# Kernel optimization log

Hardware: AMD Instinct MI355X
Metric: run time of the kernel (lower is better)

The kernel has to match this reference:

```python
import jax, jax.numpy as jnp
import numpy as np

N = 100_000
E = 1_250_000
D = 64
PAIRS = 3  # layer_num=3 -> 3 (SAGE, GIN) pairs
EPS = 1e-5


def _linear_init(key, fi, fo):
    lim = 1.0 / np.sqrt(fi)
    k1, k2 = jax.random.split(key)
    W = jax.random.uniform(k1, (fi, fo), minval=-lim, maxval=lim, dtype=jnp.float32)
    b = jax.random.uniform(k2, (fo,), minval=-lim, maxval=lim, dtype=jnp.float32)
    return W, b


def setup_inputs() -> dict:
    key = jax.random.key(0)
    ks = jax.random.split(key, 40)
    # graph
    src = jax.random.randint(ks[0], (E,), 0, N, dtype=jnp.int32)
    dst = jax.random.randint(ks[1], (E,), 0, N, dtype=jnp.int32)
    sign = (jax.random.randint(ks[2], (E,), 0, 2, dtype=jnp.int32) * 2 - 1)
    edge_index_s = jnp.stack([src, dst, sign], axis=1)  # [E,3]
    init_emb = jax.random.normal(ks[3], (N, D), dtype=jnp.float32)
    rate_b = jax.random.uniform(ks[4], (1,), dtype=jnp.float32)

    def stack_lin(kbase, fi, fo, n):
        Ws, bs = [], []
        for i in range(n):
            W, b = _linear_init(jax.random.fold_in(kbase, i), fi, fo)
            Ws.append(W); bs.append(b)
        return jnp.stack(Ws), jnp.stack(bs)

    sage_lin_W, sage_lin_b = stack_lin(ks[5], D, D, PAIRS)
    sage_norm_w = jnp.ones((PAIRS, D), jnp.float32)
    sage_norm_b = jnp.zeros((PAIRS, D), jnp.float32)
    rsW, rsB = stack_lin(ks[6], 1, D, PAIRS)   # rate_scale Linear(1,D)
    rbW, rbB = stack_lin(ks[7], 1, D, PAIRS)   # rate_bias Linear(1,D)
    sage_rs_w, sage_rs_b = rsW[:, 0, :], rsB   # [PAIRS,D]
    sage_rb_w, sage_rb_b = rbW[:, 0, :], rbB
    gin_W1, gin_b1 = stack_lin(ks[8], D, D, PAIRS)
    gin_W2, gin_b2 = stack_lin(ks[9], D, D, PAIRS)
    fuse_W, fuse_b = _linear_init(ks[10], 2 * PAIRS * D, D)
    ro_W1, ro_b1 = _linear_init(ks[11], D, 128)
    ro_W2, ro_b2 = _linear_init(ks[12], 128, 128)
    ro_W3, ro_b3 = _linear_init(ks[13], 128, 1)
    ro_ln1_g = jnp.ones((128,), jnp.float32); ro_ln1_b = jnp.zeros((128,), jnp.float32)
    ro_ln2_g = jnp.ones((128,), jnp.float32); ro_ln2_b = jnp.zeros((128,), jnp.float32)
    return dict(init_emb=init_emb, edge_index_s=edge_index_s, rate_b=rate_b,
                sage_lin_W=sage_lin_W, sage_lin_b=sage_lin_b,
                sage_norm_w=sage_norm_w, sage_norm_b=sage_norm_b,
                sage_rs_w=sage_rs_w, sage_rs_b=sage_rs_b,
                sage_rb_w=sage_rb_w, sage_rb_b=sage_rb_b,
                gin_W1=gin_W1, gin_b1=gin_b1, gin_W2=gin_W2, gin_b2=gin_b2,
                fuse_W=fuse_W, fuse_b=fuse_b,
                ro_W1=ro_W1, ro_b1=ro_b1, ro_ln1_g=ro_ln1_g, ro_ln1_b=ro_ln1_b,
                ro_W2=ro_W2, ro_b2=ro_b2, ro_ln2_g=ro_ln2_g, ro_ln2_b=ro_ln2_b,
                ro_W3=ro_W3, ro_b3=ro_b3)


def _graph_norm(x, w, b, rs_w, rs_b, rb_w, rb_b, rate):
    # batch stats over nodes (dim 0), biased variance
    mean = x.mean(0, keepdims=True)
    var = x.var(0, keepdims=True)
    x_norm = (x - mean) / jnp.sqrt(var + EPS)
    gamma = w + (rs_w * rate + rs_b)  # rate_scale(rate_b)
    beta = b + (rb_w * rate + rb_b)
    return x_norm * gamma + beta


def _layer_norm(v, g, b):
    m = v.mean(-1, keepdims=True)
    va = v.var(-1, keepdims=True)
    return (v - m) / jnp.sqrt(va + EPS) * g + b


def _forward(init_emb, edge_index_s, rate_b,
             sage_lin_W, sage_lin_b, sage_norm_w, sage_norm_b,
             sage_rs_w, sage_rs_b, sage_rb_w, sage_rb_b,
             gin_W1, gin_b1, gin_W2, gin_b2,
             fuse_W, fuse_b,
             ro_W1, ro_b1, ro_ln1_g, ro_ln1_b,
             ro_W2, ro_b2, ro_ln2_g, ro_ln2_b,
             ro_W3, ro_b3):
    n = init_emb.shape[0]
    src = edge_index_s[:, 0]
    dst = edge_index_s[:, 1]
    sign = edge_index_s[:, 2].astype(init_emb.dtype)
    rate = rate_b.reshape(())
    # degree including self-loop (for mean aggregation with fill_value=1 self loops)
    deg = jax.ops.segment_sum(jnp.ones_like(sign), dst, num_segments=n) + 1.0  # [n]
    gelu = lambda t: jax.nn.gelu(t, approximate=False)  # torch nn.GELU default = exact

    x = init_emb
    outputs = []
    for i in range(PAIRS):
        # --- StableEfficientEdgeSAGEConv (mean aggr, sign-scaled, self-loops, skip=Identity) ---
        xt = x @ sage_lin_W[i] + sage_lin_b[i]
        msg = sign[:, None] * xt[src]                                   # gather + sign scale
        agg = (jax.ops.segment_sum(msg, dst, num_segments=n) + xt) / deg[:, None]
        h = agg + x                                                     # skip (in==out -> Identity)
        h = _graph_norm(h, sage_norm_w[i], sage_norm_b[i],
                        sage_rs_w[i], sage_rs_b[i], sage_rb_w[i], sage_rb_b[i], rate)
        x = gelu(h)                                                     # dropout: eval mode (no-op)
        outputs.append(x)
        # --- GINConv (sum aggr, eps=0, no self-loops) mlp = Lin-GELU-Lin ---
        agg2 = jax.ops.segment_sum(x[src], dst, num_segments=n)
        z = x + agg2
        x = gelu(z @ gin_W1[i] + gin_b1[i]) @ gin_W2[i] + gin_b2[i]
        outputs.append(x)

    x_dense = jnp.concatenate(outputs, axis=1)          # [n, 6*D]
    x_final = x_dense @ fuse_W + fuse_b                 # [n, D]
    # readout MLP (2 hidden layers + head), eval-mode dropout
    hdd = jax.nn.relu(_layer_norm(x_final @ ro_W1 + ro_b1, ro_ln1_g, ro_ln1_b))
    hdd = jax.nn.relu(_layer_norm(hdd @ ro_W2 + ro_b2, ro_ln2_g, ro_ln2_b))
    prob = jax.nn.sigmoid(hdd @ ro_W3 + ro_b3)          # [n, 1]
    return x_final, prob


def reference(init_emb, edge_index_s, rate_b,
              sage_lin_W, sage_lin_b, sage_norm_w, sage_norm_b,
              sage_rs_w, sage_rs_b, sage_rb_w, sage_rb_b,
              gin_W1, gin_b1, gin_W2, gin_b2,
              fuse_W, fuse_b,
              ro_W1, ro_b1, ro_ln1_g, ro_ln1_b,
              ro_W2, ro_b2, ro_ln2_g, ro_ln2_b,
              ro_W3, ro_b3):
    return _forward(init_emb, edge_index_s, rate_b,
                    sage_lin_W, sage_lin_b, sage_norm_w, sage_norm_b,
                    sage_rs_w, sage_rs_b, sage_rb_w, sage_rb_b,
                    gin_W1, gin_b1, gin_W2, gin_b2,
                    fuse_W, fuse_b,
                    ro_W1, ro_b1, ro_ln1_g, ro_ln1_b,
                    ro_W2, ro_b2, ro_ln2_g, ro_ln2_b,
                    ro_W3, ro_b3)
```

## Files before the change

### kernel.cpp

```cpp
#include <hip/hip_runtime.h>
#include <hip/hip_bf16.h>
#include <math.h>


#define NBSHIFT 9
#define NBSIZE  512

__device__ __forceinline__ float gelu_f(float x) {
    return 0.5f * x * (1.0f + erff(x * 0.70710678118654752440f));
}
__device__ __forceinline__ unsigned short f2bf(float x) {
    __hip_bfloat16 h = __float2bfloat16(x);
    return *reinterpret_cast<unsigned short*>(&h);
}
__device__ __forceinline__ unsigned pack2bf(float a, float b) {
    return (unsigned)f2bf(a) | ((unsigned)f2bf(b) << 16);
}
__device__ __forceinline__ float bf2f(unsigned short u) {
    return __uint_as_float((unsigned)u << 16);
}

__global__ __launch_bounds__(256) void gemm64(
    const float* __restrict__ A,
    const float* __restrict__ Wa, const float* __restrict__ ba,
    unsigned short* __restrict__ Cb, int n)
{
    __shared__ __align__(16) float At[64][68];
    __shared__ __align__(16) float Ws[64][68];
    const int tid = threadIdx.x;
    const int tx = tid & 15, ty = tid >> 4;
    const int rowBase = blockIdx.x * 64;

    #pragma unroll
    for (int i = 0; i < 4; ++i) {
        int v  = tid + i * 256;
        int r  = v >> 4;
        int k4 = (v & 15) * 4;
        float4 a = make_float4(0.f, 0.f, 0.f, 0.f);
        int grow = rowBase + r;
        if (grow < n) a = *(const float4*)(A + (size_t)grow * 64 + k4);
        At[k4 + 0][r] = a.x; At[k4 + 1][r] = a.y;
        At[k4 + 2][r] = a.z; At[k4 + 3][r] = a.w;
        *(float4*)&Ws[r][k4] = *(const float4*)(Wa + r * 64 + k4);
    }
    __syncthreads();

    const int r0 = ty * 4, c0 = tx * 4;
    float acc[4][4];
    #pragma unroll
    for (int j = 0; j < 4; ++j) {
        float bv = ba[c0 + j];
        #pragma unroll
        for (int i = 0; i < 4; ++i) acc[i][j] = bv;
    }
    #pragma unroll 16
    for (int k = 0; k < 64; ++k) {
        float4 av = *(const float4*)&At[k][r0];
        float4 wv = *(const float4*)&Ws[k][c0];
        float a4[4] = {av.x, av.y, av.z, av.w};
        float w4[4] = {wv.x, wv.y, wv.z, wv.w};
        #pragma unroll
        for (int i = 0; i < 4; ++i)
            #pragma unroll
            for (int j = 0; j < 4; ++j)
                acc[i][j] = fmaf(a4[i], w4[j], acc[i][j]);
    }
    #pragma unroll
    for (int i = 0; i < 4; ++i) {
        int grow = rowBase + r0 + i;
        if (grow < n) {
            uint2 u;
            u.x = pack2bf(acc[i][0], acc[i][1]);
            u.y = pack2bf(acc[i][2], acc[i][3]);
            *(uint2*)(Cb + (size_t)grow * 64 + c0) = u;
        }
    }
}

template<bool FIRST>
__global__ __launch_bounds__(256) void act_fuse(
    const float* __restrict__ h,
    const float* __restrict__ colsum, const float* __restrict__ colsumsq,
    const float* __restrict__ nw, const float* __restrict__ nb,
    const float* __restrict__ rsw, const float* __restrict__ rsb,
    const float* __restrict__ rbw, const float* __restrict__ rbb,
    const float* __restrict__ rate_p, float inv_n,
    const float* __restrict__ Wf, const float* __restrict__ bf,
    unsigned short* __restrict__ xb, float* __restrict__ xfinal, int n)
{
    __shared__ __align__(16) float At[64][68];
    __shared__ __align__(16) float Ws[64][68];
    __shared__ float ab_s[128];
    const int tid = threadIdx.x;
    const int tx = tid & 15, ty = tid >> 4;
    const int rowBase = blockIdx.x * 64;

    if (tid < 64) {
        float mean = colsum[tid] * inv_n;
        float var  = colsumsq[tid] * inv_n - mean * mean;
        float rstd = rsqrtf(var + 1e-5f);
        float rate = rate_p[0];
        float gamma = nw[tid] + (rsw[tid] * rate + rsb[tid]);
        float beta  = nb[tid] + (rbw[tid] * rate + rbb[tid]);
        float a = rstd * gamma;
        ab_s[tid] = a;
        ab_s[64 + tid] = beta - mean * a;
    }
    __syncthreads();

    #pragma unroll
    for (int i = 0; i < 4; ++i) {
        int v  = tid + i * 256;
        int r  = v >> 4;
        int k4 = (v & 15) * 4;
        int grow = rowBase + r;
        float4 a = make_float4(0.f, 0.f, 0.f, 0.f);
        if (grow < n) {
            float4 hv = *(const float4*)(h + (size_t)grow * 64 + k4);
            a.x = gelu_f(fmaf(hv.x, ab_s[k4 + 0], ab_s[64 + k4 + 0]));
            a.y = gelu_f(fmaf(hv.y, ab_s[k4 + 1], ab_s[64 + k4 + 1]));
            a.z = gelu_f(fmaf(hv.z, ab_s[k4 + 2], ab_s[64 + k4 + 2]));
            a.w = gelu_f(fmaf(hv.w, ab_s[k4 + 3], ab_s[64 + k4 + 3]));
            uint2 u;
            u.x = pack2bf(a.x, a.y);
            u.y = pack2bf(a.z, a.w);
            *(uint2*)(xb + (size_t)grow * 64 + k4) = u;
        }
        At[k4 + 0][r] = a.x; At[k4 + 1][r] = a.y;
        At[k4 + 2][r] = a.z; At[k4 + 3][r] = a.w;
        *(float4*)&Ws[r][k4] = *(const float4*)(Wf + r * 64 + k4);
    }
    __syncthreads();

    const int r0 = ty * 4, c0 = tx * 4;
    float acc[4][4];
    if (FIRST) {
        #pragma unroll
        for (int j = 0; j < 4; ++j) {
            float bv = bf[c0 + j];
            #pragma unroll
            for (int i = 0; i < 4; ++i) acc[i][j] = bv;
        }
    } else {
        #pragma unroll
        for (int i = 0; i < 4; ++i)
            #pragma unroll
            for (int j = 0; j < 4; ++j) acc[i][j] = 0.f;
    }
    #pragma unroll 16
    for (int k = 0; k < 64; ++k) {
        float4 av = *(const float4*)&At[k][r0];
        float4 wv = *(const float4*)&Ws[k][c0];
        float a4[4] = {av.x, av.y, av.z, av.w};
        float w4[4] = {wv.x, wv.y, wv.z, wv.w};
        #pragma unroll
        for (int i = 0; i < 4; ++i)
            #pragma unroll
            for (int j = 0; j < 4; ++j)
                acc[i][j] = fmaf(a4[i], w4[j], acc[i][j]);
    }
    #pragma unroll
    for (int i = 0; i < 4; ++i) {
        int grow = rowBase + r0 + i;
        if (grow < n) {
            float4 r = make_float4(acc[i][0], acc[i][1], acc[i][2], acc[i][3]);
            float* cp = xfinal + (size_t)grow * 64 + c0;
            if (!FIRST) {
                float4 c = *(const float4*)cp;
                r.x += c.x; r.y += c.y; r.z += c.z; r.w += c.w;
            }
            *(float4*)cp = r;
        }
    }
}

template<bool NEXT>
__global__ __launch_bounds__(256) void gin_fuse(
    const float* __restrict__ z,
    const float* __restrict__ W1, const float* __restrict__ b1,
    const float* __restrict__ W2, const float* __restrict__ b2,
    const float* __restrict__ Wf,
    const float* __restrict__ Wn, const float* __restrict__ bn,
    float* __restrict__ xout, float* __restrict__ xfinal,
    unsigned short* __restrict__ bfout, int n)
{
    __shared__ __align__(16) float At[64][68];
    __shared__ __align__(16) float Ws[64][68];
    const int tid = threadIdx.x;
    const int tx = tid & 15, ty = tid >> 4;
    const int rowBase = blockIdx.x * 64;
    const int r0 = ty * 4, c0 = tx * 4;

    #pragma unroll
    for (int i = 0; i < 4; ++i) {
        int v  = tid + i * 256;
        int r  = v >> 4;
        int k4 = (v & 15) * 4;
        float4 a = make_float4(0.f, 0.f, 0.f, 0.f);
        int grow = rowBase + r;
        if (grow < n) a = *(const float4*)(z + (size_t)grow * 64 + k4);
        At[k4 + 0][r] = a.x; At[k4 + 1][r] = a.y;
        At[k4 + 2][r] = a.z; At[k4 + 3][r] = a.w;
        *(float4*)&Ws[r][k4] = *(const float4*)(W1 + r * 64 + k4);
    }
    __syncthreads();

    float acc[4][4];
    #pragma unroll
    for (int j = 0; j < 4; ++j) {
        float bv = b1[c0 + j];
        #pragma unroll
        for (int i = 0; i < 4; ++i) acc[i][j] = bv;
    }
    #pragma unroll 16
    for (int k = 0; k < 64; ++k) {
        float4 av = *(const float4*)&At[k][r0];
        float4 wv = *(const float4*)&Ws[k][c0];
        float a4[4] = {av.x, av.y, av.z, av.w};
        float w4[4] = {wv.x, wv.y, wv.z, wv.w};
        #pragma unroll
        for (int i = 0; i < 4; ++i)
            #pragma unroll
            for (int j = 0; j < 4; ++j)
                acc[i][j] = fmaf(a4[i], w4[j], acc[i][j]);
    }

    __syncthreads();
    #pragma unroll
    for (int i = 0; i < 4; ++i)
        #pragma unroll
        for (int j = 0; j < 4; ++j)
            At[c0 + j][r0 + i] = gelu_f(acc[i][j]);
    #pragma unroll
    for (int i = 0; i < 4; ++i) {
        int v = tid + i * 256;
        int k = v >> 4, c4 = (v & 15) * 4;
        *(float4*)&Ws[k][c4] = *(const float4*)(W2 + k * 64 + c4);
    }
    __syncthreads();
    float acc2[4][4];
    #pragma unroll
    for (int j = 0; j < 4; ++j) {
        float bv = b2[c0 + j];
        #pragma unroll
        for (int i = 0; i < 4; ++i) acc2[i][j] = bv;
    }
    #pragma unroll 16
    for (int k = 0; k < 64; ++k) {
        float4 av = *(const float4*)&At[k][r0];
        float4 wv = *(const float4*)&Ws[k][c0];
        float a4[4] = {av.x, av.y, av.z, av.w};
        float w4[4] = {wv.x, wv.y, wv.z, wv.w};
        #pragma unroll
        for (int i = 0; i < 4; ++i)
            #pragma unroll
            for (int j = 0; j < 4; ++j)
                acc2[i][j] = fmaf(a4[i], w4[j], acc2[i][j]);
    }
    #pragma unroll
    for (int i = 0; i < 4; ++i) {
        int grow = rowBase + r0 + i;
        if (grow < n)
            *(float4*)(xout + (size_t)grow * 64 + c0) =
                make_float4(acc2[i][0], acc2[i][1], acc2[i][2], acc2[i][3]);
    }

    __syncthreads();
    #pragma unroll
    for (int i = 0; i < 4; ++i)
        #pragma unroll
        for (int j = 0; j < 4; ++j)
            At[c0 + j][r0 + i] = acc2[i][j];
    #pragma unroll
    for (int i = 0; i < 4; ++i) {
        int v = tid + i * 256;
        int k = v >> 4, c4 = (v & 15) * 4;
        *(float4*)&Ws[k][c4] = *(const float4*)(Wf + k * 64 + c4);
    }
    __syncthreads();
    float acc3[4][4];
    #pragma unroll
    for (int i = 0; i < 4; ++i)
        #pragma unroll
        for (int j = 0; j < 4; ++j) acc3[i][j] = 0.f;
    #pragma unroll 16
    for (int k = 0; k < 64; ++k) {
        float4 av = *(const float4*)&At[k][r0];
        float4 wv = *(const float4*)&Ws[k][c0];
        float a4[4] = {av.x, av.y, av.z, av.w};
        float w4[4] = {wv.x, wv.y, wv.z, wv.w};
        #pragma unroll
        for (int i = 0; i < 4; ++i)
            #pragma unroll
            for (int j = 0; j < 4; ++j)
                acc3[i][j] = fmaf(a4[i], w4[j], acc3[i][j]);
    }
    #pragma unroll
    for (int i = 0; i < 4; ++i) {
        int grow = rowBase + r0 + i;
        if (grow < n) {
            float* cp = xfinal + (size_t)grow * 64 + c0;
            float4 c = *(const float4*)cp;
            c.x += acc3[i][0]; c.y += acc3[i][1];
            c.z += acc3[i][2]; c.w += acc3[i][3];
            *(float4*)cp = c;
        }
    }

    if (NEXT) {
        __syncthreads();
        #pragma unroll
        for (int i = 0; i < 4; ++i) {
            int v = tid + i * 256;
            int k = v >> 4, c4 = (v & 15) * 4;
            *(float4*)&Ws[k][c4] = *(const float4*)(Wn + k * 64 + c4);
        }
        __syncthreads();
        float acc4[4][4];
        #pragma unroll
        for (int j = 0; j < 4; ++j) {
            float bv = bn[c0 + j];
            #pragma unroll
            for (int i = 0; i < 4; ++i) acc4[i][j] = bv;
        }
        #pragma unroll 16
        for (int k = 0; k < 64; ++k) {
            float4 av = *(const float4*)&At[k][r0];
            float4 wv = *(const float4*)&Ws[k][c0];
            float a4[4] = {av.x, av.y, av.z, av.w};
            float w4[4] = {wv.x, wv.y, wv.z, wv.w};
            #pragma unroll
            for (int i = 0; i < 4; ++i)
                #pragma unroll
                for (int j = 0; j < 4; ++j)
                    acc4[i][j] = fmaf(a4[i], w4[j], acc4[i][j]);
        }
        #pragma unroll
        for (int i = 0; i < 4; ++i) {
            int grow = rowBase + r0 + i;
            if (grow < n) {
                uint2 u;
                u.x = pack2bf(acc4[i][0], acc4[i][1]);
                u.y = pack2bf(acc4[i][2], acc4[i][3]);
                *(uint2*)(bfout + (size_t)grow * 64 + c0) = u;
            }
        }
    }
}

__global__ void init_buckets(int* __restrict__ bucket_cursor, int Bn, int cap) {
    int t = threadIdx.x;
    if (t < Bn) bucket_cursor[t] = t * cap;
}

__global__ __launch_bounds__(256) void bucketA(
    const int* __restrict__ eidx, int* __restrict__ bucket_cursor,
    uint2* __restrict__ inter, int E)
{
    __shared__ int cnt[256], lo[256], cur[256], garr[256];
    __shared__ int tot_s;
    __shared__ uint2 stage[4096];
    const int tid = threadIdx.x;
    cnt[tid] = 0;
    __syncthreads();

    const int base = blockIdx.x * 4096;
    int pay[16], dfull[16];
    #pragma unroll
    for (int i = 0; i < 16; ++i) {
        int e = base + i * 256 + tid;
        dfull[i] = -1;
        if (e < E) {
            int s  = __builtin_nontemporal_load(eidx + e * 3 + 0);
            int d  = __builtin_nontemporal_load(eidx + e * 3 + 1);
            int sg = __builtin_nontemporal_load(eidx + e * 3 + 2);
            if (sg < 0) s |= 0x80000000;
            pay[i] = s;
            dfull[i] = d;
            atomicAdd(&cnt[d >> NBSHIFT], 1);
        }
    }
    __syncthreads();

    lo[tid] = cnt[tid];
    __syncthreads();
    for (int off = 1; off < 256; off <<= 1) {
        int t = (tid >= off) ? lo[tid - off] : 0;
        __syncthreads();
        lo[tid] += t;
        __syncthreads();
    }
    if (tid == 255) tot_s = lo[255];
    int excl = lo[tid] - cnt[tid];
    __syncthreads();
    lo[tid] = excl;
    cur[tid] = 0;
    if (cnt[tid] > 0) garr[tid] = atomicAdd(bucket_cursor + tid, cnt[tid]);
    __syncthreads();

    #pragma unroll
    for (int i = 0; i < 16; ++i) {
        if (dfull[i] >= 0) {
            int k = dfull[i] >> NBSHIFT;
            int r = atomicAdd(&cur[k], 1);
            stage[lo[k] + r] = make_uint2((unsigned)pay[i], (unsigned)dfull[i]);
        }
    }
    __syncthreads();

    const int tot = tot_s;
    for (int i = tid; i < tot; i += 256) {
        uint2 en = stage[i];
        int k = (int)(en.y >> NBSHIFT);
        inter[garr[k] + (i - lo[k])] = en;
    }
}

__global__ __launch_bounds__(256) void bucketB1(
    const uint2* __restrict__ inter, const int* __restrict__ bucket_cursor,
    int* __restrict__ deg_i, int cap, int n)
{
    __shared__ int cnt[NBSIZE];
    const int b = blockIdx.x, tid = threadIdx.x;
    cnt[tid] = 0; cnt[tid + 256] = 0;
    __syncthreads();
    const int base = b * cap;
    const int len = bucket_cursor[b] - base;
    for (int i = tid; i < len; i += 256)
        atomicAdd(&cnt[inter[base + i].y & (NBSIZE - 1)], 1);
    __syncthreads();
    const int nb0 = b << NBSHIFT;
    if (nb0 + tid < n)       deg_i[nb0 + tid]       = cnt[tid];
    if (nb0 + 256 + tid < n) deg_i[nb0 + 256 + tid] = cnt[256 + tid];
}

__global__ __launch_bounds__(256) void bucketB2(
    const uint2* __restrict__ inter, const int* __restrict__ bucket_cursor,
    const int* __restrict__ row_ptr, int* __restrict__ payload, int cap, int n)
{
    __shared__ int cur[NBSIZE];
    const int b = blockIdx.x, tid = threadIdx.x;
    const int nb0 = b << NBSHIFT;
    cur[tid]       = (nb0 + tid < n)       ? row_ptr[nb0 + tid]       : 0;
    cur[tid + 256] = (nb0 + 256 + tid < n) ? row_ptr[nb0 + 256 + tid] : 0;
    __syncthreads();
    const int base = b * cap;
    const int len = bucket_cursor[b] - base;
    for (int i = tid; i < len; i += 256) {
        uint2 en = inter[base + i];
        int pos = atomicAdd(&cur[en.y & (NBSIZE - 1)], 1);
        payload[pos] = (int)en.x;
    }
}

__global__ __launch_bounds__(256) void scan1(
    const int* __restrict__ deg_i, int* __restrict__ blocksum, int n, int chunk)
{
    int b = blockIdx.x;
    int lo = b * chunk, hi = min(lo + chunk, n);
    int s = 0;
    for (int i = lo + (int)threadIdx.x; i < hi; i += 256) s += deg_i[i];
    #pragma unroll
    for (int off = 32; off; off >>= 1) s += __shfl_xor(s, off, 64);
    __shared__ int ws[4];
    if ((threadIdx.x & 63) == 0) ws[threadIdx.x >> 6] = s;
    __syncthreads();
    if (threadIdx.x == 0) blocksum[b] = ws[0] + ws[1] + ws[2] + ws[3];
}

__global__ __launch_bounds__(256) void scan2(
    const int* __restrict__ blocksum, int* __restrict__ blockoff,
    int* __restrict__ row_ptr_n)
{
    int tid = threadIdx.x, lane = tid & 63, wid = tid >> 6;
    int orig = blocksum[tid];
    int v = orig;
    #pragma unroll
    for (int off = 1; off < 64; off <<= 1) {
        int t = __shfl_up(v, off, 64);
        if (lane >= off) v += t;
    }
    __shared__ int wt[4];
    if (lane == 63) wt[wid] = v;
    __syncthreads();
    int woff = 0;
    for (int w = 0; w < wid; ++w) woff += wt[w];
    blockoff[tid] = woff + v - orig;
    if (tid == 255) *row_ptr_n = woff + v;
}

__global__ __launch_bounds__(256) void scan3(
    const int* __restrict__ deg_i, const int* __restrict__ blockoff,
    int* __restrict__ row_ptr, float* __restrict__ rdeg, int n, int chunk)
{
    int b = blockIdx.x;
    int lo = b * chunk, hi = min(lo + chunk, n);
    int carry = blockoff[b];
    int tid = threadIdx.x, lane = tid & 63, wid = tid >> 6;
    __shared__ int wt[4];
    for (int base = lo; base < hi; base += 256) {
        int i = base + tid;
        int orig = (i < hi) ? deg_i[i] : 0;
        int v = orig;
        #pragma unroll
        for (int off = 1; off < 64; off <<= 1) {
            int t = __shfl_up(v, off, 64);
            if (lane >= off) v += t;
        }
        if (lane == 63) wt[wid] = v;
        __syncthreads();
        int woff = 0;
        for (int w = 0; w < wid; ++w) woff += wt[w];
        int tot = wt[0] + wt[1] + wt[2] + wt[3];
        int excl = carry + woff + (v - orig);
        if (i < hi) {
            row_ptr[i] = excl;
            rdeg[i]    = 1.0f / ((float)orig + 1.0f);
        }
        carry += tot;
        __syncthreads();
    }
}

template<bool SAGE>
__global__ __launch_bounds__(256) void gather64(
    const int* __restrict__ row_ptr, const int* __restrict__ payload,
    const unsigned short* __restrict__ valb, const float* __restrict__ xprev,
    const float* __restrict__ rdeg, float* __restrict__ out,
    float* __restrict__ colsum, float* __restrict__ colsumsq, int n)
{
    const int tid = threadIdx.x;
    const int lane = tid & 63;
    int gw = (blockIdx.x * 256 + tid) >> 6;
    int nw = (gridDim.x * 256) >> 6;
    float s = 0.f, s2 = 0.f;
    for (int node = gw; node < n; node += nw) {
        int beg = __builtin_amdgcn_readfirstlane(row_ptr[node]);
        int end = __builtin_amdgcn_readfirstlane(row_ptr[node + 1]);
        float acc = bf2f(valb[(size_t)node * 64 + lane]);
        int e = beg;
        for (; e + 8 <= end; e += 8) {
            int p0 = payload[e + 0];
            int p1 = payload[e + 1];
            int p2 = payload[e + 2];
            int p3 = payload[e + 3];
            int p4 = payload[e + 4];
            int p5 = payload[e + 5];
            int p6 = payload[e + 6];
            int p7 = payload[e + 7];
            float v0 = bf2f(valb[(size_t)(p0 & 0x7fffffff) * 64 + lane]);
            float v1 = bf2f(valb[(size_t)(p1 & 0x7fffffff) * 64 + lane]);
            float v2 = bf2f(valb[(size_t)(p2 & 0x7fffffff) * 64 + lane]);
            float v3 = bf2f(valb[(size_t)(p3 & 0x7fffffff) * 64 + lane]);
            float v4 = bf2f(valb[(size_t)(p4 & 0x7fffffff) * 64 + lane]);
            float v5 = bf2f(valb[(size_t)(p5 & 0x7fffffff) * 64 + lane]);
            float v6 = bf2f(valb[(size_t)(p6 & 0x7fffffff) * 64 + lane]);
            float v7 = bf2f(valb[(size_t)(p7 & 0x7fffffff) * 64 + lane]);
            if (SAGE) {
                v0 = (p0 < 0) ? -v0 : v0;
                v1 = (p1 < 0) ? -v1 : v1;
                v2 = (p2 < 0) ? -v2 : v2;
                v3 = (p3 < 0) ? -v3 : v3;
                v4 = (p4 < 0) ? -v4 : v4;
                v5 = (p5 < 0) ? -v5 : v5;
                v6 = (p6 < 0) ? -v6 : v6;
                v7 = (p7 < 0) ? -v7 : v7;
            }
            acc += ((v0 + v1) + (v2 + v3)) + ((v4 + v5) + (v6 + v7));
        }
        for (; e + 4 <= end; e += 4) {
            int p0 = payload[e + 0];
            int p1 = payload[e + 1];
            int p2 = payload[e + 2];
            int p3 = payload[e + 3];
            float v0 = bf2f(valb[(size_t)(p0 & 0x7fffffff) * 64 + lane]);
            float v1 = bf2f(valb[(size_t)(p1 & 0x7fffffff) * 64 + lane]);
            float v2 = bf2f(valb[(size_t)(p2 & 0x7fffffff) * 64 + lane]);
            float v3 = bf2f(valb[(size_t)(p3 & 0x7fffffff) * 64 + lane]);
            if (SAGE) {
                v0 = (p0 < 0) ? -v0 : v0;
                v1 = (p1 < 0) ? -v1 : v1;
                v2 = (p2 < 0) ? -v2 : v2;
                v3 = (p3 < 0) ? -v3 : v3;
            }
            acc += (v0 + v1) + (v2 + v3);
        }
        for (; e < end; ++e) {
            int p = payload[e];
            float v = bf2f(valb[(size_t)(p & 0x7fffffff) * 64 + lane]);
            if (SAGE) v = (p < 0) ? -v : v;
            acc += v;
        }
        float h = acc;
        if (SAGE) {
            h = fmaf(acc, rdeg[node], xprev[(size_t)node * 64 + lane]);
            s += h; s2 += h * h;
        }
        out[(size_t)node * 64 + lane] = h;
    }
    if (SAGE) {
        __shared__ float sh[2][256];
        sh[0][tid] = s; sh[1][tid] = s2;
        __syncthreads();
        if (tid < 64) {
            float a = sh[0][tid] + sh[0][tid + 64] + sh[0][tid + 128] + sh[0][tid + 192];
            float b = sh[1][tid] + sh[1][tid + 64] + sh[1][tid + 128] + sh[1][tid + 192];
            atomicAdd(colsum + tid, a);
            atomicAdd(colsumsq + tid, b);
        }
    }
}

__global__ __launch_bounds__(256) void readout1(
    const float* __restrict__ xf, const float* __restrict__ W1,
    const float* __restrict__ b1, const float* __restrict__ g1,
    const float* __restrict__ bt1, float* __restrict__ H, int n)
{
    __shared__ __align__(16) float At[64][68];
    __shared__ __align__(16) float Ws[64][132];
    const int tid = threadIdx.x;
    const int tx = tid & 15, ty = tid >> 4;
    const int rowBase = blockIdx.x * 64;

    #pragma unroll
    for (int i = 0; i < 4; ++i) {
        int v = tid + i * 256;
        int r = v >> 4, k4 = (v & 15) * 4;
        float4 a = make_float4(0.f, 0.f, 0.f, 0.f);
        int grow = rowBase + r;
        if (grow < n) a = *(const float4*)(xf + (size_t)grow * 64 + k4);
        At[k4 + 0][r] = a.x; At[k4 + 1][r] = a.y;
        At[k4 + 2][r] = a.z; At[k4 + 3][r] = a.w;
    }
    #pragma unroll
    for (int i = 0; i < 8; ++i) {
        int v = tid + i * 256;
        int k = v >> 5, c4 = (v & 31) * 4;
        *(float4*)&Ws[k][c4] = *(const float4*)(W1 + k * 128 + c4);
    }
    __syncthreads();

    const int r0 = ty * 4, c0 = tx * 8;
    float acc[4][8];
    #pragma unroll
    for (int j = 0; j < 8; ++j) {
        float bv = b1[c0 + j];
        #pragma unroll
        for (int i = 0; i < 4; ++i) acc[i][j] = bv;
    }
    #pragma unroll 8
    for (int k = 0; k < 64; ++k) {
        float4 av = *(const float4*)&At[k][r0];
        float4 w0 = *(const float4*)&Ws[k][c0];
        float4 w1v = *(const float4*)&Ws[k][c0 + 4];
        float a4[4] = {av.x, av.y, av.z, av.w};
        float w8[8] = {w0.x, w0.y, w0.z, w0.w, w1v.x, w1v.y, w1v.z, w1v.w};
        #pragma unroll
        for (int i = 0; i < 4; ++i)
            #pragma unroll
            for (int j = 0; j < 8; ++j)
                acc[i][j] = fmaf(a4[i], w8[j], acc[i][j]);
    }

    float gj[8], bj[8];
    #pragma unroll
    for (int j = 0; j < 8; ++j) { gj[j] = g1[c0 + j]; bj[j] = bt1[c0 + j]; }
    #pragma unroll
    for (int i = 0; i < 4; ++i) {
        int grow = rowBase + r0 + i;
        float s = 0.f, s2 = 0.f;
        #pragma unroll
        for (int j = 0; j < 8; ++j) { s += acc[i][j]; s2 += acc[i][j] * acc[i][j]; }
        #pragma unroll
        for (int off = 8; off; off >>= 1) {
            s  += __shfl_xor(s, off, 16);
            s2 += __shfl_xor(s2, off, 16);
        }
        float mean = s * (1.f / 128.f);
        float var  = s2 * (1.f / 128.f) - mean * mean;
        float rstd = rsqrtf(var + 1e-5f);
        float o[8];
        #pragma unroll
        for (int j = 0; j < 8; ++j)
            o[j] = fmaxf(fmaf((acc[i][j] - mean) * rstd, gj[j], bj[j]), 0.f);
        if (grow < n) {
            *(float4*)(H + (size_t)grow * 128 + c0)     = make_float4(o[0], o[1], o[2], o[3]);
            *(float4*)(H + (size_t)grow * 128 + c0 + 4) = make_float4(o[4], o[5], o[6], o[7]);
        }
    }
}

__global__ __launch_bounds__(256) void readout2(
    const float* __restrict__ H, const float* __restrict__ W2,
    const float* __restrict__ b2, const float* __restrict__ g2,
    const float* __restrict__ bt2, const float* __restrict__ W3,
    const float* __restrict__ b3, float* __restrict__ prob, int n)
{
    __shared__ __align__(16) float Ht[64][68];
    __shared__ __align__(16) float Ws[64][132];
    const int tid = threadIdx.x;
    const int tx = tid & 15, ty = tid >> 4;
    const int rowBase = blockIdx.x * 64;
    const int r0 = ty * 4, c0 = tx * 8;

    float acc[4][8];
    #pragma unroll
    for (int j = 0; j < 8; ++j) {
        float bv = b2[c0 + j];
        #pragma unroll
        for (int i = 0; i < 4; ++i) acc[i][j] = bv;
    }

    for (int kc = 0; kc < 2; ++kc) {
        if (kc) __syncthreads();
        #pragma unroll
        for (int i = 0; i < 4; ++i) {
            int v = tid + i * 256;
            int r = v >> 4, k4 = (v & 15) * 4;
            float4 a = make_float4(0.f, 0.f, 0.f, 0.f);
            int grow = rowBase + r;
            if (grow < n) a = *(const float4*)(H + (size_t)grow * 128 + kc * 64 + k4);
            Ht[k4 + 0][r] = a.x; Ht[k4 + 1][r] = a.y;
            Ht[k4 + 2][r] = a.z; Ht[k4 + 3][r] = a.w;
        }
        #pragma unroll
        for (int i = 0; i < 8; ++i) {
            int v = tid + i * 256;
            int k = v >> 5, c4 = (v & 31) * 4;
            *(float4*)&Ws[k][c4] = *(const float4*)(W2 + (kc * 64 + k) * 128 + c4);
        }
        __syncthreads();
        #pragma unroll 8
        for (int k = 0; k < 64; ++k) {
            float4 av = *(const float4*)&Ht[k][r0];
            float4 w0 = *(const float4*)&Ws[k][c0];
            float4 w1v = *(const float4*)&Ws[k][c0 + 4];
            float a4[4] = {av.x, av.y, av.z, av.w};
            float w8[8] = {w0.x, w0.y, w0.z, w0.w, w1v.x, w1v.y, w1v.z, w1v.w};
            #pragma unroll
            for (int i = 0; i < 4; ++i)
                #pragma unroll
                for (int j = 0; j < 8; ++j)
                    acc[i][j] = fmaf(a4[i], w8[j], acc[i][j]);
        }
    }

    float gj[8], bj[8], w3[8];
    #pragma unroll
    for (int j = 0; j < 8; ++j) {
        gj[j] = g2[c0 + j]; bj[j] = bt2[c0 + j]; w3[j] = W3[c0 + j];
    }
    const float bias3 = b3[0];
    #pragma unroll
    for (int i = 0; i < 4; ++i) {
        int grow = rowBase + r0 + i;
        float s = 0.f, s2 = 0.f;
        #pragma unroll
        for (int j = 0; j < 8; ++j) { s += acc[i][j]; s2 += acc[i][j] * acc[i][j]; }
        #pragma unroll
        for (int off = 8; off; off >>= 1) {
            s  += __shfl_xor(s, off, 16);
            s2 += __shfl_xor(s2, off, 16);
        }
        float mean = s * (1.f / 128.f);
        float var  = s2 * (1.f / 128.f) - mean * mean;
        float rstd = rsqrtf(var + 1e-5f);
        float d = 0.f;
        #pragma unroll
        for (int j = 0; j < 8; ++j) {
            float v = fmaxf(fmaf((acc[i][j] - mean) * rstd, gj[j], bj[j]), 0.f);
            d = fmaf(v, w3[j], d);
        }
        #pragma unroll
        for (int off = 8; off; off >>= 1) d += __shfl_xor(d, off, 16);
        if (tx == 0 && grow < n)
            prob[grow] = 1.f / (1.f + expf(-(d + bias3)));
    }
}

extern "C" void kernel_launch(void* const* d_in, const int* in_sizes, int n_in,
                              void* d_out, int out_size, void* d_ws, size_t ws_size,
                              hipStream_t stream)
{
    const float* init_emb = (const float*)d_in[0];
    const int*   eidx     = (const int*)d_in[1];
    const float* rate_b   = (const float*)d_in[2];
    const float* sage_W   = (const float*)d_in[3];
    const float* sage_b   = (const float*)d_in[4];
    const float* norm_w   = (const float*)d_in[5];
    const float* norm_b   = (const float*)d_in[6];
    const float* rs_w     = (const float*)d_in[7];
    const float* rs_b     = (const float*)d_in[8];
    const float* rb_w     = (const float*)d_in[9];
    const float* rb_b     = (const float*)d_in[10];
    const float* gin_W1   = (const float*)d_in[11];
    const float* gin_b1   = (const float*)d_in[12];
    const float* gin_W2   = (const float*)d_in[13];
    const float* gin_b2   = (const float*)d_in[14];
    const float* fuse_W   = (const float*)d_in[15];
    const float* fuse_b   = (const float*)d_in[16];
    const float* ro_W1    = (const float*)d_in[17];
    const float* ro_b1    = (const float*)d_in[18];
    const float* ln1_g    = (const float*)d_in[19];
    const float* ln1_b    = (const float*)d_in[20];
    const float* ro_W2    = (const float*)d_in[21];
    const float* ro_b2    = (const float*)d_in[22];
    const float* ln2_g    = (const float*)d_in[23];
    const float* ln2_b    = (const float*)d_in[24];
    const float* ro_W3    = (const float*)d_in[25];
    const float* ro_b3    = (const float*)d_in[26];

    const int N = in_sizes[0] / 64;
    const int E = in_sizes[1] / 3;
    const size_t nf = (size_t)N * 64;

    float* bufA  = (float*)d_ws;
    float* bufB  = bufA + nf;
    float* bufC  = bufB + nf;
    unsigned short* bfbuf = (unsigned short*)(bufC + nf);
    float* rdeg  = (float*)(bfbuf + nf);
    float* stats = rdeg + N;
    int*   row_ptr  = (int*)(stats + 3 * 256);
    int*   deg_i    = row_ptr + (N + 1);
    int*   blocksum = deg_i + N;
    int*   blockoff = blocksum + 256;
    int*   bucket_cursor = blockoff + 256;
    int*   payload  = bucket_cursor + 256;
    uint2* inter    = (uint2*)bufC;

    float* xfinal = (float*)d_out;
    float* prob   = xfinal + nf;
    float* H      = bufA;

    const int gemm_blocks = (N + 63) / 64;
    const int gather_blocks = 2048;
    const int chunk  = (N + 255) / 256;
    const float inv_n = 1.0f / (float)N;

    const int Bn   = (N + NBSIZE - 1) / NBSIZE;
    const int meanb = (E + Bn - 1) / Bn;
    const int cap  = meanb + meanb / 8 + 64;
    const int ablocks = (E + 4095) / 4096;

    hipMemsetAsync(stats, 0, 3 * 256 * sizeof(float), stream);
    init_buckets<<<1, 256, 0, stream>>>(bucket_cursor, Bn, cap);
    bucketA<<<ablocks, 256, 0, stream>>>(eidx, bucket_cursor, inter, E);
    bucketB1<<<Bn, 256, 0, stream>>>(inter, bucket_cursor, deg_i, cap, N);
    scan1<<<256, 256, 0, stream>>>(deg_i, blocksum, N, chunk);
    scan2<<<1, 256, 0, stream>>>(blocksum, blockoff, row_ptr + N);
    scan3<<<256, 256, 0, stream>>>(deg_i, blockoff, row_ptr, rdeg, N, chunk);
    bucketB2<<<Bn, 256, 0, stream>>>(inter, bucket_cursor, row_ptr, payload, cap, N);

    for (int p = 0; p < 3; ++p) {
        const float* Xp = (p == 0) ? init_emb : (p == 1 ? (const float*)bufB : (const float*)bufC);
        float* B2p = (p == 1) ? bufC : bufB;
        float* cs = stats + p * 256;

        if (p == 0)
            gemm64<<<gemm_blocks, 256, 0, stream>>>(
                Xp, sage_W, sage_b, bfbuf, N);
        gather64<true><<<gather_blocks, 256, 0, stream>>>(
            row_ptr, payload, bfbuf, Xp, rdeg, B2p, cs, cs + 64, N);
        if (p == 0)
            act_fuse<true><<<gemm_blocks, 256, 0, stream>>>(
                B2p, cs, cs + 64,
                norm_w + p * 64, norm_b + p * 64, rs_w + p * 64, rs_b + p * 64,
                rb_w + p * 64, rb_b + p * 64, rate_b, inv_n,
                fuse_W, fuse_b, bfbuf, xfinal, N);
        else
            act_fuse<false><<<gemm_blocks, 256, 0, stream>>>(
                B2p, cs, cs + 64,
                norm_w + p * 64, norm_b + p * 64, rs_w + p * 64, rs_b + p * 64,
                rb_w + p * 64, rb_b + p * 64, rate_b, inv_n,
                fuse_W + (2 * p) * 4096, nullptr, bfbuf, xfinal, N);
        gather64<false><<<gather_blocks, 256, 0, stream>>>(
            row_ptr, payload, bfbuf, nullptr, nullptr, B2p, nullptr, nullptr, N);
        if (p < 2)
            gin_fuse<true><<<gemm_blocks, 256, 0, stream>>>(
                B2p, gin_W1 + p * 4096, gin_b1 + p * 64,
                gin_W2 + p * 4096, gin_b2 + p * 64,
                fuse_W + (2 * p + 1) * 4096,
                sage_W + (p + 1) * 4096, sage_b + (p + 1) * 64,
                B2p, xfinal, bfbuf, N);
        else
            gin_fuse<false><<<gemm_blocks, 256, 0, stream>>>(
                B2p, gin_W1 + p * 4096, gin_b1 + p * 64,
                gin_W2 + p * 4096, gin_b2 + p * 64,
                fuse_W + (2 * p + 1) * 4096,
                nullptr, nullptr, B2p, xfinal, nullptr, N);
    }

    readout1<<<gemm_blocks, 256, 0, stream>>>(
        xfinal, ro_W1, ro_b1, ln1_g, ln1_b, H, N);
    readout2<<<gemm_blocks, 256, 0, stream>>>(
        H, ro_W2, ro_b2, ln2_g, ln2_b, ro_W3, ro_b3, prob, N);
}
```

Measured before the change: 867.8 us.

## Gather 8 neighbors per wavefront with 16-byte vector loads and shuffle reduction

Restructures the neighbor-gather kernel so each wavefront splits into 8 sub-groups. Each sub-group loads one neighbor's full 64-dim bf16 row as 8-lane uint4 vector loads, and the next payload indices are software-prefetched. Partial sums are then combined across sub-groups with xor shuffles. This replaces the per-lane 2-byte scalar loads with wide loads and raises the number of independent row fetches in flight, targeting the latency-bound random gather. The cost is extra shuffle reduction work, lanes doing masked dummy loads when degree is not a multiple of 16, and only 8 lanes active for the epilogue and store.

```diff
diff --git a/kernel.cpp b/kernel.cpp
--- a/kernel.cpp
+++ b/kernel.cpp
@@ -522,6 +522,17 @@
     }
 }
 
+__device__ __forceinline__ void accum8(float* a, uint4 u, float s) {
+    a[0] = fmaf(__uint_as_float(u.x << 16),          s, a[0]);
+    a[1] = fmaf(__uint_as_float(u.x & 0xffff0000u),  s, a[1]);
+    a[2] = fmaf(__uint_as_float(u.y << 16),          s, a[2]);
+    a[3] = fmaf(__uint_as_float(u.y & 0xffff0000u),  s, a[3]);
+    a[4] = fmaf(__uint_as_float(u.z << 16),          s, a[4]);
+    a[5] = fmaf(__uint_as_float(u.z & 0xffff0000u),  s, a[5]);
+    a[6] = fmaf(__uint_as_float(u.w << 16),          s, a[6]);
+    a[7] = fmaf(__uint_as_float(u.w & 0xffff0000u),  s, a[7]);
+}
+
 template<bool SAGE>
 __global__ __launch_bounds__(256) void gather64(
     const int* __restrict__ row_ptr, const int* __restrict__ payload,
@@ -529,84 +540,104 @@
     const float* __restrict__ rdeg, float* __restrict__ out,
     float* __restrict__ colsum, float* __restrict__ colsumsq, int n)
 {
-    const int tid = threadIdx.x;
+    const int tid  = threadIdx.x;
     const int lane = tid & 63;
+    const int sub  = lane >> 3;
+    const int c0   = (lane & 7) * 8;
+    const int wid  = tid >> 6;
     int gw = (blockIdx.x * 256 + tid) >> 6;
     int nw = (gridDim.x * 256) >> 6;
-    float s = 0.f, s2 = 0.f;
+
+    float st[8], st2[8];
+    if (SAGE) {
+        #pragma unroll
+        for (int j = 0; j < 8; ++j) { st[j] = 0.f; st2[j] = 0.f; }
+    }
+
     for (int node = gw; node < n; node += nw) {
         int beg = __builtin_amdgcn_readfirstlane(row_ptr[node]);
         int end = __builtin_amdgcn_readfirstlane(row_ptr[node + 1]);
-        float acc = bf2f(valb[(size_t)node * 64 + lane]);
-        int e = beg;
-        for (; e + 8 <= end; e += 8) {
-            int p0 = payload[e + 0];
-            int p1 = payload[e + 1];
-            int p2 = payload[e + 2];
-            int p3 = payload[e + 3];
-            int p4 = payload[e + 4];
-            int p5 = payload[e + 5];
-            int p6 = payload[e + 6];
-            int p7 = payload[e + 7];
-            float v0 = bf2f(valb[(size_t)(p0 & 0x7fffffff) * 64 + lane]);
-            float v1 = bf2f(valb[(size_t)(p1 & 0x7fffffff) * 64 + lane]);
-            float v2 = bf2f(valb[(size_t)(p2 & 0x7fffffff) * 64 + lane]);
-            float v3 = bf2f(valb[(size_t)(p3 & 0x7fffffff) * 64 + lane]);
-            float v4 = bf2f(valb[(size_t)(p4 & 0x7fffffff) * 64 + lane]);
-            float v5 = bf2f(valb[(size_t)(p5 & 0x7fffffff) * 64 + lane]);
-            float v6 = bf2f(valb[(size_t)(p6 & 0x7fffffff) * 64 + lane]);
-            float v7 = bf2f(valb[(size_t)(p7 & 0x7fffffff) * 64 + lane]);
+
+        float a[8];
+        #pragma unroll
+        for (int j = 0; j < 8; ++j) a[j] = 0.f;
+
+        int i0 = beg + sub, i1 = beg + 8 + sub;
+        bool v0 = i0 < end, v1 = i1 < end;
+        int p0 = v0 ? payload[i0] : 0;
+        int p1 = v1 ? payload[i1] : 0;
+
+        for (int e = beg; e < end; e += 16) {
+            int  q0 = p0,  q1 = p1;
+            bool w0 = v0,  w1 = v1;
+            int ni0 = e + 16 + sub, ni1 = e + 24 + sub;
+            v0 = ni0 < end; v1 = ni1 < end;
+            p0 = v0 ? payload[ni0] : 0;
+            p1 = v1 ? payload[ni1] : 0;
+
+            int r0 = w0 ? (q0 & 0x7fffffff) : node;
+            int r1 = w1 ? (q1 & 0x7fffffff) : node;
+            uint4 u0 = *(const uint4*)(valb + (size_t)r0 * 64 + c0);
+            uint4 u1 = *(const uint4*)(valb + (size_t)r1 * 64 + c0);
+            float s0 = w0 ? ((SAGE && q0 < 0) ? -1.f : 1.f) : 0.f;
+            float s1 = w1 ? ((SAGE && q1 < 0) ? -1.f : 1.f) : 0.f;
+            accum8(a, u0, s0);
+            accum8(a, u1, s1);
+        }
+
+        #pragma unroll
+        for (int j = 0; j < 8; ++j) {
+            a[j] += __shfl_xor(a[j], 8, 64);
+            a[j] += __shfl_xor(a[j], 16, 64);
+            a[j] += __shfl_xor(a[j], 32, 64);
+        }
+
+        if (sub == 0) {
+            uint4 us = *(const uint4*)(valb + (size_t)node * 64 + c0);
+            a[0] += __uint_as_float(us.x << 16);
+            a[1] += __uint_as_float(us.x & 0xffff0000u);
+            a[2] += __uint_as_float(us.y << 16);
+            a[3] += __uint_as_float(us.y & 0xffff0000u);
+            a[4] += __uint_as_float(us.z << 16);
+            a[5] += __uint_as_float(us.z & 0xffff0000u);
+            a[6] += __uint_as_float(us.w << 16);
+            a[7] += __uint_as_float(us.w & 0xffff0000u);
             if (SAGE) {
-                v0 = (p0 < 0) ? -v0 : v0;
-                v1 = (p1 < 0) ? -v1 : v1;
-                v2 = (p2 < 0) ? -v2 : v2;
-                v3 = (p3 < 0) ? -v3 : v3;
-                v4 = (p4 < 0) ? -v4 : v4;
-                v5 = (p5 < 0) ? -v5 : v5;
-                v6 = (p6 < 0) ? -v6 : v6;
-                v7 = (p7 < 0) ? -v7 : v7;
+                float rd = rdeg[node];
+                float4 xp0 = *(const float4*)(xprev + (size_t)node * 64 + c0);
+                float4 xp1 = *(const float4*)(xprev + (size_t)node * 64 + c0 + 4);
+                float xp[8] = {xp0.x, xp0.y, xp0.z, xp0.w,
+                               xp1.x, xp1.y, xp1.z, xp1.w};
+                #pragma unroll
+                for (int j = 0; j < 8; ++j) {
+                    float h = fmaf(a[j], rd, xp[j]);
+                    st[j]  += h;
+                    st2[j] += h * h;
+                    a[j] = h;
+                }
             }
-            acc += ((v0 + v1) + (v2 + v3)) + ((v4 + v5) + (v6 + v7));
-        }
-        for (; e + 4 <= end; e += 4) {
-            int p0 = payload[e + 0];
-            int p1 = payload[e + 1];
-            int p2 = payload[e + 2];
-            int p3 = payload[e + 3];
-            float v0 = bf2f(valb[(size_t)(p0 & 0x7fffffff) * 64 + lane]);
-            float v1 = bf2f(valb[(size_t)(p1 & 0x7fffffff) * 64 + lane]);
-            float v2 = bf2f(valb[(size_t)(p2 & 0x7fffffff) * 64 + lane]);
-            float v3 = bf2f(valb[(size_t)(p3 & 0x7fffffff) * 64 + lane]);
-            if (SAGE) {
-                v0 = (p0 < 0) ? -v0 : v0;
-                v1 = (p1 < 0) ? -v1 : v1;
-                v2 = (p2 < 0) ? -v2 : v2;
-                v3 = (p3 < 0) ? -v3 : v3;
+            *(float4*)(out + (size_t)node * 64 + c0) =
+                make_float4(a[0], a[1], a[2], a[3]);
+            *(float4*)(out + (size_t)node * 64 + c0 + 4) =
+                make_float4(a[4], a[5], a[6], a[7]);
+        }
+    }
+
+    if (SAGE) {
+        __shared__ float sh[2][4][64];
+        if (sub == 0) {
+            #pragma unroll
+            for (int j = 0; j < 8; ++j) {
+                sh[0][wid][c0 + j] = st[j];
+                sh[1][wid][c0 + j] = st2[j];
             }
-            acc += (v0 + v1) + (v2 + v3);
-        }
-        for (; e < end; ++e) {
-            int p = payload[e];
-            float v = bf2f(valb[(size_t)(p & 0x7fffffff) * 64 + lane]);
-            if (SAGE) v = (p < 0) ? -v : v;
-            acc += v;
-        }
-        float h = acc;
-        if (SAGE) {
-            h = fmaf(acc, rdeg[node], xprev[(size_t)node * 64 + lane]);
-            s += h; s2 += h * h;
-        }
-        out[(size_t)node * 64 + lane] = h;
-    }
-    if (SAGE) {
-        __shared__ float sh[2][256];
-        sh[0][tid] = s; sh[1][tid] = s2;
+        }
         __syncthreads();
         if (tid < 64) {
-            float a = sh[0][tid] + sh[0][tid + 64] + sh[0][tid + 128] + sh[0][tid + 192];
-            float b = sh[1][tid] + sh[1][tid + 64] + sh[1][tid + 128] + sh[1][tid + 192];
-            atomicAdd(colsum + tid, a);
-            atomicAdd(colsumsq + tid, b);
+            float a_ = sh[0][0][tid] + sh[0][1][tid] + sh[0][2][tid] + sh[0][3][tid];
+            float b_ = sh[1][0][tid] + sh[1][1][tid] + sh[1][2][tid] + sh[1][3][tid];
+            atomicAdd(colsum + tid, a_);
+            atomicAdd(colsumsq + tid, b_);
         }
     }
 }
```

Result: slower. 919.0 us (+5.9%).
